# Performance work log

Hardware: AMD Instinct MI355X
Metric: run time of the kernel (lower is better)

Reference implementation:

```python
import jax, jax.numpy as jnp
import numpy as np
import math

D_MODEL, N_HEADS, D_HEAD = 768, 12, 64
INIT_RANGE = 0.02
ROPE_BASE = 10000.0


def _rope_cos_sin(seq_len, d_head, dtype=jnp.float32):
    # theta_j = base^(-2j/d), positions m -> angles [T, d/2]
    inv_freq = 1.0 / (ROPE_BASE ** (jnp.arange(0, d_head, 2, dtype=jnp.float32) / d_head))
    ang = jnp.arange(seq_len, dtype=jnp.float32)[:, None] * inv_freq[None, :]
    return jnp.cos(ang).astype(dtype), jnp.sin(ang).astype(dtype)


def _apply_rope(x, cos, sin):
    # x: [b, t, h, d]; rotate consecutive (even, odd) pairs as complex numbers
    xr, xi = x[..., 0::2], x[..., 1::2]
    c = cos[None, :, None, :]
    s = sin[None, :, None, :]
    out_r = xr * c - xi * s
    out_i = xr * s + xi * c
    return jnp.stack([out_r, out_i], axis=-1).reshape(x.shape)


def setup_inputs() -> dict:
    key = jax.random.key(0)
    ks = jax.random.split(key, 5)
    B, T = 2, 2048
    x = jax.random.normal(ks[0], (B, T, D_MODEL), dtype=jnp.float32)
    W_Q = INIT_RANGE * jax.random.normal(ks[1], (N_HEADS, D_MODEL, D_HEAD), dtype=jnp.float32)
    W_K = INIT_RANGE * jax.random.normal(ks[2], (N_HEADS, D_MODEL, D_HEAD), dtype=jnp.float32)
    W_V = INIT_RANGE * jax.random.normal(ks[3], (N_HEADS, D_MODEL, D_HEAD), dtype=jnp.float32)
    W_O = INIT_RANGE * jax.random.normal(ks[4], (N_HEADS, D_HEAD, D_MODEL), dtype=jnp.float32)
    b_Q = jnp.zeros((N_HEADS, D_HEAD), dtype=jnp.float32)
    b_K = jnp.zeros((N_HEADS, D_HEAD), dtype=jnp.float32)
    b_V = jnp.zeros((N_HEADS, D_HEAD), dtype=jnp.float32)
    b_O = jnp.zeros((D_MODEL,), dtype=jnp.float32)
    return {"normalized_resid_pre": x, "W_Q": W_Q, "b_Q": b_Q, "W_K": W_K, "b_K": b_K,
            "W_V": W_V, "b_V": b_V, "W_O": W_O, "b_O": b_O}


def reference(normalized_resid_pre, W_Q, b_Q, W_K, b_K, W_V, b_V, W_O, b_O):
    x = normalized_resid_pre
    B, T, _ = x.shape
    cos, sin = _rope_cos_sin(T, D_HEAD, x.dtype)
    Q = jnp.einsum('btc,hcd->bthd', x, W_Q) + b_Q
    K = jnp.einsum('btc,hcd->bthd', x, W_K) + b_K
    V = jnp.einsum('btc,hcd->bthd', x, W_V) + b_V
    Q = _apply_rope(Q, cos, sin)
    K = _apply_rope(K, cos, sin)
    scores = jnp.einsum('bqhd,bkhd->bhqk', Q, K) / math.sqrt(D_HEAD)
    # Faithful to source: tril zeros upper triangle, then all exact zeros -> -inf
    tril = jnp.tril(jnp.ones((T, T), dtype=bool))
    z = jnp.where(tril[None, None], scores, 0.0)
    z = jnp.where(z == 0.0, -jnp.inf, z)
    probs = jax.nn.softmax(z, axis=-1)
    o = jnp.einsum('bhqk,bkhd->bqhd', probs, V)
    return jnp.einsum('bqhd,hdm->bqm', o, W_O) + b_O
```

## Files before the change

kernel.cpp:

```cpp
#include <hip/hip_runtime.h>

typedef unsigned short u16;
typedef unsigned int u32;
typedef short bf16x8 __attribute__((ext_vector_type(8)));
typedef float f32x4 __attribute__((ext_vector_type(4)));
typedef float f32x16 __attribute__((ext_vector_type(16)));

#define MFMA(a, b, c) __builtin_amdgcn_mfma_f32_16x16x32_bf16(a, b, c, 0, 0, 0)
#define MFMA32(a, b, c) __builtin_amdgcn_mfma_f32_32x32x16_bf16(a, b, c, 0, 0, 0)

__device__ __forceinline__ u16 f2bf(float f) {
  unsigned int u = __float_as_uint(f);
  u = (u + 0x7FFFu + ((u >> 16) & 1u)) >> 16;
  return (u16)u;
}

#define GLOAD16(gp, lp)                                                        \
  __builtin_amdgcn_global_load_lds(                                            \
      (const __attribute__((address_space(1))) void*)(gp),                     \
      (__attribute__((address_space(3))) void*)(lp), 16, 0, 0)

__global__ __launch_bounds__(256) void prep_all(
    const float* __restrict__ x, const float* __restrict__ WQ,
    const float* __restrict__ WK, const float* __restrict__ WV,
    const float* __restrict__ WO, float* __restrict__ cost, float* __restrict__ sint,
    u16* __restrict__ xb, u16* __restrict__ Wt, u16* __restrict__ WoT) {
  __shared__ float tile[32][33];
  const int bid = blockIdx.x, tid = threadIdx.x;

  if (bid < 256) {
    int idx = bid * 256 + tid;
    int t = idx >> 5, i = idx & 31;
    float invf = expf(-(float)i * 0.28782313662425572f);
    float ang = (float)t * invf;
    cost[idx] = cosf(ang);
    sint[idx] = sinf(ang);
  } else if (bid < 3328) {
    int i = ((bid - 256) * 256 + tid) * 4;
    float4 v = *(const float4*)(x + i);
    ushort4 o = make_ushort4(f2bf(v.x), f2bf(v.y), f2bf(v.z), f2bf(v.w));
    *(ushort4*)(xb + i) = o;
  } else if (bid < 5056) {
    const int pbid = bid - 3328;
    const int z = pbid / 48, rem = pbid - z * 48;
    const int y = rem / 24, xk = rem - y * 24;
    const int qkv = z / 12, h = z - qkv * 12;
    const float* W = (qkv == 0 ? WQ : qkv == 1 ? WK : WV) + (size_t)h * 768 * 64;
    const int k0 = xk * 32, d0 = y * 32;
    const int tx = tid & 31, ty = tid >> 5;
#pragma unroll
    for (int it = 0; it < 4; it++)
      tile[ty + it * 8][tx] = W[(size_t)(k0 + ty + it * 8) * 64 + d0 + tx];
    __syncthreads();
    u16* out = Wt + (size_t)(qkv * 768 + h * 64 + d0) * 768 + k0;
#pragma unroll
    for (int it = 0; it < 4; it++)
      out[(size_t)(ty + it * 8) * 768 + tx] = f2bf(tile[tx][ty + it * 8]);
  } else {
    const int wbid = bid - 5056;
    const int a0 = (wbid % 24) * 32, m0 = (wbid / 24) * 32;
    const int tx = tid & 31, ty = tid >> 5;
#pragma unroll
    for (int it = 0; it < 4; it++)
      tile[ty + it * 8][tx] = WO[(size_t)(a0 + ty + it * 8) * 768 + m0 + tx];
    __syncthreads();
#pragma unroll
    for (int it = 0; it < 4; it++)
      WoT[(size_t)(m0 + ty + it * 8) * 768 + a0 + tx] = f2bf(tile[tx][ty + it * 8]);
  }
}

template <int MODE>
__global__ __launch_bounds__(256) void gemm_bt(
    const u16* __restrict__ A, const u16* __restrict__ Bt, int K, int LDA, int LDB,
    const float* __restrict__ bQ, const float* __restrict__ bK, const float* __restrict__ bV,
    const float* __restrict__ cost, const float* __restrict__ sint,
    u16* __restrict__ Qb, u16* __restrict__ Kb, u16* __restrict__ Vt,
    const float* __restrict__ bO, float* __restrict__ Out) {
  __shared__ u16 As[3][64 * 32];
  __shared__ u16 Bs[3][128 * 32];
  const int tid = threadIdx.x;
  const int w = tid >> 6, l = tid & 63;
  const int lr = l >> 4, lc = l & 15;
  const int wr = w >> 1, wc = w & 1;

  const int id = blockIdx.x;
  const int xcd = id & 7, idx = id >> 3;
  const int m0 = (xcd * 8 + (idx & 7)) * 64;
  const int n0 = (idx >> 3) * 128;

  f32x4 acc[2][4];
#pragma unroll
  for (int mi = 0; mi < 2; mi++)
#pragma unroll
    for (int ni = 0; ni < 4; ni++) acc[mi][ni] = (f32x4){0.f, 0.f, 0.f, 0.f};

  const int srow = w * 16 + (l >> 2);
  const int sg = (l & 3) ^ ((l >> 3) & 3);
  const u16* ga = A + (size_t)(m0 + srow) * LDA + sg * 8;
  const u16* gb = Bt + (size_t)(n0 + srow) * LDB + sg * 8;

#define GSTAGE(t, bi)                                                   \
  {                                                                     \
    const int kk = (t) * 32;                                            \
    GLOAD16(ga + kk, &As[bi][w * 512]);                                 \
    GLOAD16(gb + kk, &Bs[bi][w * 512]);                                 \
    GLOAD16(gb + kk + (size_t)64 * LDB, &Bs[bi][2048 + w * 512]);       \
  }

  const int n = K >> 5;
  GSTAGE(0, 0);
  if (n > 1) GSTAGE(1, 1);

  for (int kt = 0; kt < n; kt++) {
    if (kt + 1 < n) asm volatile("s_waitcnt vmcnt(3)" ::: "memory");
    else            asm volatile("s_waitcnt vmcnt(0)" ::: "memory");
    __builtin_amdgcn_s_barrier();
    __builtin_amdgcn_sched_barrier(0);
    if (kt + 2 < n) GSTAGE(kt + 2, (kt + 2) % 3);

    const char* as = (const char*)As[kt % 3];
    const char* bs = (const char*)Bs[kt % 3];
    bf16x8 af[2], bfr[4];
#pragma unroll
    for (int mi = 0; mi < 2; mi++) {
      const int row = wr * 32 + mi * 16 + lc;
      af[mi] = *(const bf16x8*)(as + row * 64 + ((lr ^ ((row >> 1) & 3)) << 4));
    }
#pragma unroll
    for (int ni = 0; ni < 4; ni++) {
      const int row = wc * 64 + ni * 16 + lc;
      bfr[ni] = *(const bf16x8*)(bs + row * 64 + ((lr ^ ((row >> 1) & 3)) << 4));
    }
    __builtin_amdgcn_s_setprio(1);
#pragma unroll
    for (int mi = 0; mi < 2; mi++)
#pragma unroll
      for (int ni = 0; ni < 4; ni++)
        acc[mi][ni] = MFMA(af[mi], bfr[ni], acc[mi][ni]);
    __builtin_amdgcn_s_setprio(0);
  }
#undef GSTAGE

#pragma unroll
  for (int mi = 0; mi < 2; mi++) {
#pragma unroll
    for (int ni = 0; ni < 4; ni++) {
      const int col = n0 + wc * 64 + ni * 16 + lc;
      const int rowb = m0 + wr * 32 + mi * 16 + lr * 4;
      if (MODE == 0) {
        const int qkv = col / 768;
        const int rem = col - qkv * 768;
        const int h = rem >> 6, d = rem & 63, fi = d >> 1;
        const float bb = (qkv == 0 ? bQ : qkv == 1 ? bK : bV)[rem];
#pragma unroll
        for (int r = 0; r < 4; r++) {
          const int grow = rowb + r;
          const int t = grow & 2047;
          float v = acc[mi][ni][r] + bb;
          float pv = __shfl_xor(v, 1);
          if (qkv < 2) {
            const float c = cost[t * 32 + fi], s = sint[t * 32 + fi];
            float o = (d & 1) ? (pv * s + v * c) : (v * c - pv * s);
            if (qkv == 0) o *= 0.125f;
            (qkv == 0 ? Qb : Kb)[(size_t)grow * 768 + rem] = f2bf(o);
          } else {
            const int bidx = grow >> 11;
            Vt[((size_t)(bidx * 12 + h) * 64 + d) * 2048 + t] = f2bf(v);
          }
        }
      } else {
        const float bb = bO[col];
#pragma unroll
        for (int r = 0; r < 4; r++) {
          const int grow = rowb + r;
          Out[(size_t)grow * 768 + col] = acc[mi][ni][r] + bb;
        }
      }
    }
  }
}

__global__ __launch_bounds__(256, 2) void attn_kernel(
    const u16* __restrict__ Qb, const u16* __restrict__ Kb,
    const u16* __restrict__ Vt, u16* __restrict__ Ob) {
  __shared__ char Kls[4][8192];
  __shared__ char Vls[4][8192];
  char* scratch = (char*)Kls;

  const int id = blockIdx.x + 16 * blockIdx.y;
  const int s_ = id >> 3;
  const int bh = (id & 7) + 8 * (s_ % 3);
  const int xq = s_ / 3;
  const int b = bh / 12, h = bh - b * 12;
  const int tid = threadIdx.x, w = tid >> 6, l = tid & 63;
  const int lq = l & 31, hi = l >> 5;
  const int qhalf = w & 1, grp = w >> 1;

  const u16* kbase = Kb + (size_t)(b * 2048) * 768 + h * 64;
  const u16* vbase = Vt + (size_t)(bh * 64) * 2048;

  const int r8 = l >> 3;
  const int scol8 = (l & 7) ^ r8;
  const u16* ksrc = kbase + (size_t)(w * 16 + r8) * 768 + scol8 * 8;
  const u16* vsrc = vbase + (size_t)(w * 16 + r8) * 2048 + scol8 * 8;

#define STAGE(t, bi)                                                        \
  {                                                                         \
    const size_t ko = (size_t)(t) * 64 * 768;                               \
    const int vo = (t) * 64;                                                \
    GLOAD16(ksrc + ko,            &Kls[bi][w * 2048]);                      \
    GLOAD16(ksrc + ko + 8 * 768,  &Kls[bi][w * 2048 + 1024]);               \
    GLOAD16(vsrc + vo,            &Vls[bi][w * 2048]);                      \
    GLOAD16(vsrc + vo + 8 * 2048, &Vls[bi][w * 2048 + 1024]);               \
  }

  const int fswz = (lq & 7) << 4;

#pragma unroll 1
  for (int half = 0; half < 2; half++) {
    const int qblk = half == 0 ? 31 - xq : xq;
    const int n = qblk + 1;
    const int nsup = (n + 1) >> 1;

    bf16x8 qf[4];
    {
      const u16* qp = Qb + ((size_t)(b * 2048 + qblk * 64 + qhalf * 32 + lq)) * 768 +
                      h * 64 + hi * 8;
#pragma unroll
      for (int c = 0; c < 4; c++) qf[c] = *(const bf16x8*)(qp + c * 16);
    }

    float m_run = -INFINITY, l_run = 0.f;
    f32x16 acc2[2];
    acc2[0] = (f32x16)0.0f;
    acc2[1] = (f32x16)0.0f;

    STAGE(0, 0);
    if (n > 1) STAGE(1, 1);

    for (int p = 0; p < nsup; p++) {
      const int t0 = 2 * p;
      asm volatile("s_waitcnt vmcnt(0)" ::: "memory");
      __builtin_amdgcn_s_barrier();
      __builtin_amdgcn_sched_barrier(0);
      if (t0 + 2 < n) STAGE(t0 + 2, (t0 + 2) & 3);
      if (t0 + 3 < n) STAGE(t0 + 3, (t0 + 3) & 3);

      const int tile = t0 + grp;
      if (tile < n) {
        const int cur = tile & 3;

        f32x16 s2[2];
        s2[0] = (f32x16)0.0f;
        s2[1] = (f32x16)0.0f;
        __builtin_amdgcn_s_setprio(1);
#pragma unroll
        for (int c = 0; c < 4; c++) {
          const int cb = (c * 32 + hi * 16) ^ fswz;
          bf16x8 kf0 = *(const bf16x8*)(&Kls[cur][lq * 128] + cb);
          bf16x8 kf1 = *(const bf16x8*)(&Kls[cur][(32 + lq) * 128] + cb);
          s2[0] = MFMA32(kf0, qf[c], s2[0]);
          s2[1] = MFMA32(kf1, qf[c], s2[1]);
        }
        __builtin_amdgcn_s_setprio(0);

        if (tile == qblk) {
          const int qrel = qhalf * 32 + lq;
#pragma unroll
          for (int kt2 = 0; kt2 < 2; kt2++)
#pragma unroll
            for (int r = 0; r < 16; r++) {
              const int ko = kt2 * 32 + (r & 3) + 8 * (r >> 2) + 4 * hi;
              if (ko > qrel) s2[kt2][r] = -INFINITY;
            }
        }

        float pm = s2[0][0];
#pragma unroll
        for (int r = 1; r < 16; r++) pm = fmaxf(pm, s2[0][r]);
#pragma unroll
        for (int r = 0; r < 16; r++) pm = fmaxf(pm, s2[1][r]);
        pm = fmaxf(pm, __shfl_xor(pm, 32));

        const float mn = fmaxf(m_run, pm);
        const float alpha = __expf(m_run - mn);
        m_run = mn;

        float rs = 0.f;
        u32 pk[2][8];
#pragma unroll
        for (int kt2 = 0; kt2 < 2; kt2++)
#pragma unroll
          for (int j = 0; j < 8; j++) {
            float p0 = __expf(s2[kt2][2 * j] - mn);
            float p1 = __expf(s2[kt2][2 * j + 1] - mn);
            rs += p0 + p1;
            asm("v_cvt_pk_bf16_f32 %0, %1, %2" : "=v"(pk[kt2][j]) : "v"(p0), "v"(p1));
          }
        l_run = l_run * alpha + rs;

        union { u32 u[4]; bf16x8 v; } pf[4];
#pragma unroll
        for (int kq = 0; kq < 4; kq++) {
          const int kt2 = kq >> 1, i0 = 4 * (kq & 1);
          u32 a0 = pk[kt2][i0], b0 = pk[kt2][i0 + 2];
          u32 a1 = pk[kt2][i0 + 1], b1 = pk[kt2][i0 + 3];
          asm("v_permlane32_swap_b32 %0, %1" : "+v"(a0), "+v"(b0));
          asm("v_permlane32_swap_b32 %0, %1" : "+v"(a1), "+v"(b1));
          pf[kq].u[0] = a0; pf[kq].u[1] = a1; pf[kq].u[2] = b0; pf[kq].u[3] = b1;
        }

#pragma unroll
        for (int dh = 0; dh < 2; dh++)
#pragma unroll
          for (int r = 0; r < 16; r++) acc2[dh][r] *= alpha;

        __builtin_amdgcn_s_setprio(1);
#pragma unroll
        for (int dh = 0; dh < 2; dh++) {
          const char* vr = &Vls[cur][(dh * 32 + lq) * 128];
#pragma unroll
          for (int kq = 0; kq < 4; kq++) {
            bf16x8 vf = *(const bf16x8*)(vr + ((kq * 32 + hi * 16) ^ fswz));
            acc2[dh] = MFMA32(vf, pf[kq].v, acc2[dh]);
          }
        }
        __builtin_amdgcn_s_setprio(0);
      }
    }

    asm volatile("s_waitcnt lgkmcnt(0)" ::: "memory");
    __builtin_amdgcn_s_barrier();
    if (grp == 1) {
      float* sc = (float*)scratch + ((size_t)(w - 2) * 64 + l) * 34;
#pragma unroll
      for (int dh = 0; dh < 2; dh++)
#pragma unroll
        for (int r = 0; r < 16; r++) sc[dh * 16 + r] = acc2[dh][r];
      sc[32] = m_run;
      sc[33] = l_run;
    }
    asm volatile("s_waitcnt lgkmcnt(0)" ::: "memory");
    __builtin_amdgcn_s_barrier();
    if (grp == 0) {
      const float* sc = (const float*)scratch + ((size_t)w * 64 + l) * 34;
      const float m1 = sc[32], l1 = sc[33];
      const float M = fmaxf(m_run, m1);
      const float a0 = __expf(m_run - M);
      const float a1 = __expf(m1 - M);
      const float lm = l_run * a0 + l1 * a1;
      const float lt = lm + __shfl_xor(lm, 32);
      const float inv = 1.0f / lt;
      u16* ob = Ob + ((size_t)(b * 2048 + qblk * 64 + qhalf * 32 + lq)) * 768 + h * 64;
#pragma unroll
      for (int dh = 0; dh < 2; dh++)
#pragma unroll
        for (int g = 0; g < 4; g++) {
          ushort4 o4;
          o4.x = f2bf((acc2[dh][4 * g + 0] * a0 + sc[dh * 16 + 4 * g + 0] * a1) * inv);
          o4.y = f2bf((acc2[dh][4 * g + 1] * a0 + sc[dh * 16 + 4 * g + 1] * a1) * inv);
          o4.z = f2bf((acc2[dh][4 * g + 2] * a0 + sc[dh * 16 + 4 * g + 2] * a1) * inv);
          o4.w = f2bf((acc2[dh][4 * g + 3] * a0 + sc[dh * 16 + 4 * g + 3] * a1) * inv);
          *(ushort4*)(ob + dh * 32 + 8 * g + 4 * hi) = o4;
        }
    }
    asm volatile("s_waitcnt lgkmcnt(0)" ::: "memory");
    __builtin_amdgcn_s_barrier();
  }
#undef STAGE
}


extern "C" void kernel_launch(void* const* d_in, const int* in_sizes, int n_in,
                              void* d_out, int out_size, void* d_ws, size_t ws_size,
                              hipStream_t stream) {
  const float* x  = (const float*)d_in[0];
  const float* WQ = (const float*)d_in[1];
  const float* bQ = (const float*)d_in[2];
  const float* WK = (const float*)d_in[3];
  const float* bK = (const float*)d_in[4];
  const float* WV = (const float*)d_in[5];
  const float* bV = (const float*)d_in[6];
  const float* WO = (const float*)d_in[7];
  const float* bO = (const float*)d_in[8];

  char* ws = (char*)d_ws;
  u16* Xb    = (u16*)(ws + 0);
  u16* Wqkv  = (u16*)(ws + 6291456);
  u16* WoT   = (u16*)(ws + 9830400);
  u16* Qb    = (u16*)(ws + 11010048);
  u16* Kb    = (u16*)(ws + 17301504);
  u16* Vt    = (u16*)(ws + 23592960);
  u16* Ob    = (u16*)(ws + 29884416);
  float* cost = (float*)(ws + 36175872);
  float* sint = (float*)(ws + 36438016);

  prep_all<<<5632, 256, 0, stream>>>(x, WQ, WK, WV, WO, cost, sint, Xb, Wqkv, WoT);

  gemm_bt<0><<<1152, 256, 0, stream>>>(Xb, Wqkv, 768, 768, 768,
                                       bQ, bK, bV, cost, sint,
                                       Qb, Kb, Vt, nullptr, nullptr);
  attn_kernel<<<dim3(16, 24), 256, 0, stream>>>(Qb, Kb, Vt, Ob);
  gemm_bt<1><<<384, 256, 0, stream>>>(Ob, WoT, 768, 768, 768,
                                      nullptr, nullptr, nullptr, nullptr, nullptr,
                                      nullptr, nullptr, nullptr, bO, (float*)d_out);
}
```

Baseline: 107.3 us.

## Use 128x128 GEMM tiles with split-K across two wave groups

```diff
diff --git a/kernel.cpp b/kernel.cpp
--- a/kernel.cpp
+++ b/kernel.cpp
@@ -71,60 +71,63 @@
 }
 
 template <int MODE>
-__global__ __launch_bounds__(256) void gemm_bt(
+__global__ __launch_bounds__(512, 4) void gemm_bt(
     const u16* __restrict__ A, const u16* __restrict__ Bt, int K, int LDA, int LDB,
     const float* __restrict__ bQ, const float* __restrict__ bK, const float* __restrict__ bV,
     const float* __restrict__ cost, const float* __restrict__ sint,
     u16* __restrict__ Qb, u16* __restrict__ Kb, u16* __restrict__ Vt,
     const float* __restrict__ bO, float* __restrict__ Out) {
-  __shared__ u16 As[3][64 * 32];
-  __shared__ u16 Bs[3][128 * 32];
+  __shared__ u16 SH[32768];
+#define AS_(bi) (&SH[(bi) * 8192])
+#define BS_(bi) (&SH[(bi) * 8192 + 4096])
   const int tid = threadIdx.x;
   const int w = tid >> 6, l = tid & 63;
+  const int grp = w >> 2, wsub = w & 3;
   const int lr = l >> 4, lc = l & 15;
-  const int wr = w >> 1, wc = w & 1;
+  const int wr = wsub >> 1, wc = wsub & 1;
 
   const int id = blockIdx.x;
   const int xcd = id & 7, idx = id >> 3;
-  const int m0 = (xcd * 8 + (idx & 7)) * 64;
-  const int n0 = (idx >> 3) * 128;
-
-  f32x4 acc[2][4];
-#pragma unroll
-  for (int mi = 0; mi < 2; mi++)
+  const int m0 = (xcd * 4 + (idx & 3)) * 128;
+  const int n0 = (idx >> 2) * 128;
+
+  f32x4 acc[4][4];
+#pragma unroll
+  for (int mi = 0; mi < 4; mi++)
 #pragma unroll
     for (int ni = 0; ni < 4; ni++) acc[mi][ni] = (f32x4){0.f, 0.f, 0.f, 0.f};
 
-  const int srow = w * 16 + (l >> 2);
-  const int sg = (l & 3) ^ ((l >> 3) & 3);
+  const int srow = tid >> 2;
+  const int sg = (tid & 3) ^ ((tid >> 3) & 3);
   const u16* ga = A + (size_t)(m0 + srow) * LDA + sg * 8;
   const u16* gb = Bt + (size_t)(n0 + srow) * LDB + sg * 8;
 
 #define GSTAGE(t, bi)                                                   \
   {                                                                     \
     const int kk = (t) * 32;                                            \
-    GLOAD16(ga + kk, &As[bi][w * 512]);                                 \
-    GLOAD16(gb + kk, &Bs[bi][w * 512]);                                 \
-    GLOAD16(gb + kk + (size_t)64 * LDB, &Bs[bi][2048 + w * 512]);       \
-  }
-
-  const int n = K >> 5;
+    GLOAD16(ga + kk, &AS_(bi)[w * 512]);                                \
+    GLOAD16(gb + kk, &BS_(bi)[w * 512]);                                \
+  }
+
+  const int nt = K >> 5;
+  const int nsup = nt >> 1;
   GSTAGE(0, 0);
-  if (n > 1) GSTAGE(1, 1);
-
-  for (int kt = 0; kt < n; kt++) {
-    if (kt + 1 < n) asm volatile("s_waitcnt vmcnt(3)" ::: "memory");
-    else            asm volatile("s_waitcnt vmcnt(0)" ::: "memory");
+  GSTAGE(1, 1);
+
+  for (int p = 0; p < nsup; p++) {
+    asm volatile("s_waitcnt vmcnt(0)" ::: "memory");
     __builtin_amdgcn_s_barrier();
     __builtin_amdgcn_sched_barrier(0);
-    if (kt + 2 < n) GSTAGE(kt + 2, (kt + 2) % 3);
-
-    const char* as = (const char*)As[kt % 3];
-    const char* bs = (const char*)Bs[kt % 3];
-    bf16x8 af[2], bfr[4];
-#pragma unroll
-    for (int mi = 0; mi < 2; mi++) {
-      const int row = wr * 32 + mi * 16 + lc;
+    if (2 * p + 2 < nt) GSTAGE(2 * p + 2, (2 * p + 2) & 3);
+    if (2 * p + 3 < nt) GSTAGE(2 * p + 3, (2 * p + 3) & 3);
+
+    const int tile = 2 * p + grp;
+    const char* as = (const char*)AS_(tile & 3);
+    const char* bs = (const char*)BS_(tile & 3);
+    bf16x8 af[4], bfr[4];
+#pragma unroll
+    for (int mi = 0; mi < 4; mi++) {
+      const int row = wr * 64 + mi * 16 + lc;
       af[mi] = *(const bf16x8*)(as + row * 64 + ((lr ^ ((row >> 1) & 3)) << 4));
     }
 #pragma unroll
@@ -134,7 +137,7 @@
     }
     __builtin_amdgcn_s_setprio(1);
 #pragma unroll
-    for (int mi = 0; mi < 2; mi++)
+    for (int mi = 0; mi < 4; mi++)
 #pragma unroll
       for (int ni = 0; ni < 4; ni++)
         acc[mi][ni] = MFMA(af[mi], bfr[ni], acc[mi][ni]);
@@ -142,43 +145,68 @@
   }
 #undef GSTAGE
 
-#pragma unroll
-  for (int mi = 0; mi < 2; mi++) {
-#pragma unroll
-    for (int ni = 0; ni < 4; ni++) {
-      const int col = n0 + wc * 64 + ni * 16 + lc;
-      const int rowb = m0 + wr * 32 + mi * 16 + lr * 4;
-      if (MODE == 0) {
-        const int qkv = col / 768;
-        const int rem = col - qkv * 768;
-        const int h = rem >> 6, d = rem & 63, fi = d >> 1;
-        const float bb = (qkv == 0 ? bQ : qkv == 1 ? bK : bV)[rem];
-#pragma unroll
-        for (int r = 0; r < 4; r++) {
-          const int grow = rowb + r;
-          const int t = grow & 2047;
-          float v = acc[mi][ni][r] + bb;
-          float pv = __shfl_xor(v, 1);
-          if (qkv < 2) {
-            const float c = cost[t * 32 + fi], s = sint[t * 32 + fi];
-            float o = (d & 1) ? (pv * s + v * c) : (v * c - pv * s);
-            if (qkv == 0) o *= 0.125f;
-            (qkv == 0 ? Qb : Kb)[(size_t)grow * 768 + rem] = f2bf(o);
-          } else {
-            const int bidx = grow >> 11;
-            Vt[((size_t)(bidx * 12 + h) * 64 + d) * 2048 + t] = f2bf(v);
+  asm volatile("s_waitcnt vmcnt(0)" ::: "memory");
+  __builtin_amdgcn_s_barrier();
+  float* sc = (float*)SH;
+  const int t8 = (wsub << 6) | l;
+  if (grp == 1) {
+#pragma unroll
+    for (int mi = 0; mi < 4; mi++)
+#pragma unroll
+      for (int ni = 0; ni < 4; ni++)
+        *(f32x4*)((char*)sc + (mi * 4 + ni) * 4096 + t8 * 16) = acc[mi][ni];
+  }
+  asm volatile("s_waitcnt lgkmcnt(0)" ::: "memory");
+  __builtin_amdgcn_s_barrier();
+  if (grp == 0) {
+#pragma unroll
+    for (int mi = 0; mi < 4; mi++)
+#pragma unroll
+      for (int ni = 0; ni < 4; ni++) {
+        f32x4 o = *(const f32x4*)((const char*)sc + (mi * 4 + ni) * 4096 + t8 * 16);
+        acc[mi][ni] += o;
+      }
+
+#pragma unroll
+    for (int mi = 0; mi < 4; mi++) {
+#pragma unroll
+      for (int ni = 0; ni < 4; ni++) {
+        const int col = n0 + wc * 64 + ni * 16 + lc;
+        const int rowb = m0 + wr * 64 + mi * 16 + lr * 4;
+        if (MODE == 0) {
+          const int qkv = col / 768;
+          const int rem = col - qkv * 768;
+          const int h = rem >> 6, d = rem & 63, fi = d >> 1;
+          const float bb = (qkv == 0 ? bQ : qkv == 1 ? bK : bV)[rem];
+#pragma unroll
+          for (int r = 0; r < 4; r++) {
+            const int grow = rowb + r;
+            const int t = grow & 2047;
+            float v = acc[mi][ni][r] + bb;
+            float pv = __shfl_xor(v, 1);
+            if (qkv < 2) {
+              const float c = cost[t * 32 + fi], s = sint[t * 32 + fi];
+              float o = (d & 1) ? (pv * s + v * c) : (v * c - pv * s);
+              if (qkv == 0) o *= 0.125f;
+              (qkv == 0 ? Qb : Kb)[(size_t)grow * 768 + rem] = f2bf(o);
+            } else {
+              const int bidx = grow >> 11;
+              Vt[((size_t)(bidx * 12 + h) * 64 + d) * 2048 + t] = f2bf(v);
+            }
           }
-        }
-      } else {
-        const float bb = bO[col];
-#pragma unroll
-        for (int r = 0; r < 4; r++) {
-          const int grow = rowb + r;
-          Out[(size_t)grow * 768 + col] = acc[mi][ni][r] + bb;
+        } else {
+          const float bb = bO[col];
+#pragma unroll
+          for (int r = 0; r < 4; r++) {
+            const int grow = rowb + r;
+            Out[(size_t)grow * 768 + col] = acc[mi][ni][r] + bb;
+          }
         }
       }
     }
   }
+#undef AS_
+#undef BS_
 }
 
 __global__ __launch_bounds__(256, 2) void attn_kernel(
@@ -398,11 +426,11 @@
 
   prep_all<<<5632, 256, 0, stream>>>(x, WQ, WK, WV, WO, cost, sint, Xb, Wqkv, WoT);
 
-  gemm_bt<0><<<1152, 256, 0, stream>>>(Xb, Wqkv, 768, 768, 768,
-                                       bQ, bK, bV, cost, sint,
-                                       Qb, Kb, Vt, nullptr, nullptr);
+  gemm_bt<0><<<576, 512, 0, stream>>>(Xb, Wqkv, 768, 768, 768,
+                                      bQ, bK, bV, cost, sint,
+                                      Qb, Kb, Vt, nullptr, nullptr);
   attn_kernel<<<dim3(16, 24), 256, 0, stream>>>(Qb, Kb, Vt, Ob);
-  gemm_bt<1><<<384, 256, 0, stream>>>(Ob, WoT, 768, 768, 768,
+  gemm_bt<1><<<192, 512, 0, stream>>>(Ob, WoT, 768, 768, 768,
                                       nullptr, nullptr, nullptr, nullptr, nullptr,
                                       nullptr, nullptr, nullptr, bO, (float*)d_out);
 }
```

New measurement: 105.9 us. About the same (-1.3%).

## Enlarge GEMM tiles to 128x128x64 with double buffering

Applied to the files above, without the earlier changes.

```diff
diff --git a/kernel.cpp b/kernel.cpp
--- a/kernel.cpp
+++ b/kernel.cpp
@@ -77,8 +77,8 @@
     const float* __restrict__ cost, const float* __restrict__ sint,
     u16* __restrict__ Qb, u16* __restrict__ Kb, u16* __restrict__ Vt,
     const float* __restrict__ bO, float* __restrict__ Out) {
-  __shared__ u16 As[3][64 * 32];
-  __shared__ u16 Bs[3][128 * 32];
+  __shared__ u16 As[2][128 * 64];
+  __shared__ u16 Bs[2][128 * 64];
   const int tid = threadIdx.x;
   const int w = tid >> 6, l = tid & 63;
   const int lr = l >> 4, lc = l & 15;
@@ -86,68 +86,74 @@
 
   const int id = blockIdx.x;
   const int xcd = id & 7, idx = id >> 3;
-  const int m0 = (xcd * 8 + (idx & 7)) * 64;
-  const int n0 = (idx >> 3) * 128;
-
-  f32x4 acc[2][4];
-#pragma unroll
-  for (int mi = 0; mi < 2; mi++)
+  const int m0 = (xcd * 4 + (idx & 3)) * 128;
+  const int n0 = (idx >> 2) * 128;
+
+  f32x4 acc[4][4];
+#pragma unroll
+  for (int mi = 0; mi < 4; mi++)
 #pragma unroll
     for (int ni = 0; ni < 4; ni++) acc[mi][ni] = (f32x4){0.f, 0.f, 0.f, 0.f};
 
-  const int srow = w * 16 + (l >> 2);
-  const int sg = (l & 3) ^ ((l >> 3) & 3);
+  const int srow = w * 8 + (l >> 3);
+  const int sg = (l & 7) ^ (l >> 3);
   const u16* ga = A + (size_t)(m0 + srow) * LDA + sg * 8;
   const u16* gb = Bt + (size_t)(n0 + srow) * LDB + sg * 8;
 
-#define GSTAGE(t, bi)                                                   \
-  {                                                                     \
-    const int kk = (t) * 32;                                            \
-    GLOAD16(ga + kk, &As[bi][w * 512]);                                 \
-    GLOAD16(gb + kk, &Bs[bi][w * 512]);                                 \
-    GLOAD16(gb + kk + (size_t)64 * LDB, &Bs[bi][2048 + w * 512]);       \
-  }
-
-  const int n = K >> 5;
+#define GSTAGE(t, bi)                                                       \
+  {                                                                         \
+    const int kk = (t) * 64;                                                \
+    _Pragma("unroll")                                                       \
+    for (int i = 0; i < 4; i++) {                                           \
+      GLOAD16(ga + (size_t)(i * 32) * LDA + kk, &As[bi][i * 2048 + w * 512]); \
+      GLOAD16(gb + (size_t)(i * 32) * LDB + kk, &Bs[bi][i * 2048 + w * 512]); \
+    }                                                                       \
+  }
+
+  const int nt = K >> 6;
   GSTAGE(0, 0);
-  if (n > 1) GSTAGE(1, 1);
-
-  for (int kt = 0; kt < n; kt++) {
-    if (kt + 1 < n) asm volatile("s_waitcnt vmcnt(3)" ::: "memory");
-    else            asm volatile("s_waitcnt vmcnt(0)" ::: "memory");
+
+  for (int kt = 0; kt < nt; kt++) {
+    asm volatile("s_waitcnt vmcnt(0)" ::: "memory");
     __builtin_amdgcn_s_barrier();
     __builtin_amdgcn_sched_barrier(0);
-    if (kt + 2 < n) GSTAGE(kt + 2, (kt + 2) % 3);
-
-    const char* as = (const char*)As[kt % 3];
-    const char* bs = (const char*)Bs[kt % 3];
-    bf16x8 af[2], bfr[4];
-#pragma unroll
-    for (int mi = 0; mi < 2; mi++) {
-      const int row = wr * 32 + mi * 16 + lc;
-      af[mi] = *(const bf16x8*)(as + row * 64 + ((lr ^ ((row >> 1) & 3)) << 4));
+    if (kt + 1 < nt) GSTAGE(kt + 1, (kt + 1) & 1);
+
+    const char* as = (const char*)As[kt & 1];
+    const char* bs = (const char*)Bs[kt & 1];
+    bf16x8 af[4][2], bfr[4][2];
+#pragma unroll
+    for (int mi = 0; mi < 4; mi++) {
+      const int row = wr * 64 + mi * 16 + lc;
+#pragma unroll
+      for (int ks = 0; ks < 2; ks++)
+        af[mi][ks] = *(const bf16x8*)(as + row * 128 + (((ks * 4 + lr) ^ (lc & 7)) << 4));
     }
 #pragma unroll
     for (int ni = 0; ni < 4; ni++) {
       const int row = wc * 64 + ni * 16 + lc;
-      bfr[ni] = *(const bf16x8*)(bs + row * 64 + ((lr ^ ((row >> 1) & 3)) << 4));
+#pragma unroll
+      for (int ks = 0; ks < 2; ks++)
+        bfr[ni][ks] = *(const bf16x8*)(bs + row * 128 + (((ks * 4 + lr) ^ (lc & 7)) << 4));
     }
     __builtin_amdgcn_s_setprio(1);
 #pragma unroll
-    for (int mi = 0; mi < 2; mi++)
-#pragma unroll
-      for (int ni = 0; ni < 4; ni++)
-        acc[mi][ni] = MFMA(af[mi], bfr[ni], acc[mi][ni]);
+    for (int ks = 0; ks < 2; ks++)
+#pragma unroll
+      for (int mi = 0; mi < 4; mi++)
+#pragma unroll
+        for (int ni = 0; ni < 4; ni++)
+          acc[mi][ni] = MFMA(af[mi][ks], bfr[ni][ks], acc[mi][ni]);
     __builtin_amdgcn_s_setprio(0);
   }
 #undef GSTAGE
 
 #pragma unroll
-  for (int mi = 0; mi < 2; mi++) {
+  for (int mi = 0; mi < 4; mi++) {
 #pragma unroll
     for (int ni = 0; ni < 4; ni++) {
       const int col = n0 + wc * 64 + ni * 16 + lc;
-      const int rowb = m0 + wr * 32 + mi * 16 + lr * 4;
+      const int rowb = m0 + wr * 64 + mi * 16 + lr * 4;
       if (MODE == 0) {
         const int qkv = col / 768;
         const int rem = col - qkv * 768;
@@ -398,11 +404,11 @@
 
   prep_all<<<5632, 256, 0, stream>>>(x, WQ, WK, WV, WO, cost, sint, Xb, Wqkv, WoT);
 
-  gemm_bt<0><<<1152, 256, 0, stream>>>(Xb, Wqkv, 768, 768, 768,
-                                       bQ, bK, bV, cost, sint,
-                                       Qb, Kb, Vt, nullptr, nullptr);
+  gemm_bt<0><<<576, 256, 0, stream>>>(Xb, Wqkv, 768, 768, 768,
+                                      bQ, bK, bV, cost, sint,
+                                      Qb, Kb, Vt, nullptr, nullptr);
   attn_kernel<<<dim3(16, 24), 256, 0, stream>>>(Qb, Kb, Vt, Ob);
-  gemm_bt<1><<<384, 256, 0, stream>>>(Ob, WoT, 768, 768, 768,
+  gemm_bt<1><<<192, 256, 0, stream>>>(Ob, WoT, 768, 768, 768,
                                       nullptr, nullptr, nullptr, nullptr, nullptr,
                                       nullptr, nullptr, nullptr, bO, (float*)d_out);
 }
```

Result: slower. 109.4 us (+2.0%).
